# Optimization experiments

Hardware: AMD Instinct MI355X
Metric: run time of the kernel (lower is better)

## Reference

```python
import jax, jax.numpy as jnp
import numpy as np
from jax import lax

N = 64            # n_channels
L = 5             # n_layers
CLS = 12          # n_classes
B = 262144        # batch
NUM_MZI = N * (N - 1) // 2
C_HALF = 0.7071067811865476  # sqrt(0.5)
RESP = 0.8        # photodiode_responsivity
SENS = 0.001      # sensitivity
GAMMA = 0.05      # fwhm / 2

# MZI pair indices in the same order as the torch double loop (i, then j>i)
_II, _JJ = np.triu_indices(N, k=1)
_II = jnp.asarray(_II, dtype=jnp.int32)
_JJ = jnp.asarray(_JJ, dtype=jnp.int32)


def construct_unitary(mzi_phases, output_phases):
    # mzi_phases: [NUM_MZI*2] interleaved (theta, phi); output_phases: [N]
    thetas = mzi_phases[0::2]
    phis = mzi_phases[1::2]

    def step(U, inp):
        i, j, theta, phi = inp
        ui = U[i]
        uj = U[j]
        e_phi = jnp.exp(1j * phi)
        e_theta = jnp.exp(1j * theta)
        new_i = C_HALF * ui + C_HALF * e_phi * uj
        new_j = C_HALF * e_theta * ui - C_HALF * e_theta * e_phi * uj
        U = U.at[i].set(new_i).at[j].set(new_j)
        return U, None

    U0 = jnp.eye(N, dtype=jnp.complex64)
    U, _ = lax.scan(step, U0, (_II, _JJ, thetas, phis))
    # output phase screen: diag(exp(i*phase)) @ U
    return jnp.exp(1j * output_phases)[:, None] * U


def nofu(field, beta_param, initial_detuning):
    beta = jax.nn.sigmoid(beta_param)                       # [N]
    input_power = jnp.abs(field) ** 2                       # [B, N]
    detuning = initial_detuning + SENS * RESP * beta * input_power
    transmission = GAMMA / (GAMMA + 1j * detuning)          # complex Lorentzian
    return jnp.sqrt(jax.nn.relu(1.0 - beta)) * field * transmission


def setup_inputs() -> dict:
    key = jax.random.key(0)
    ks = jax.random.split(key, 12)
    return {
        "x": jax.random.normal(ks[0], (B, N), dtype=jnp.float32),
        "mzi_phases": 0.1 * jax.random.normal(ks[1], (L, NUM_MZI * 2), dtype=jnp.float32),
        "output_phases": 0.1 * jax.random.normal(ks[2], (L, N), dtype=jnp.float32),
        "beta_param": 0.1 * jax.random.normal(ks[3], (L - 1, N), dtype=jnp.float32),
        "initial_detuning": 0.1 * jax.random.normal(ks[4], (L - 1, N), dtype=jnp.float32),
        "W1": 0.1 * jax.random.normal(ks[5], (2 * N, N), dtype=jnp.float32),
        "b1": jnp.zeros((2 * N,), dtype=jnp.float32),
        "W2": 0.1 * jax.random.normal(ks[6], (N, 2 * N), dtype=jnp.float32),
        "b2": jnp.zeros((N,), dtype=jnp.float32),
        "W3": 0.1 * jax.random.normal(ks[7], (CLS, N), dtype=jnp.float32),
        "b3": jnp.zeros((CLS,), dtype=jnp.float32),
    }


def reference(x, mzi_phases, output_phases, beta_param, initial_detuning,
              W1, b1, W2, b2, W3, b3):
    field = x.astype(jnp.complex64)                         # [B, N]
    for l in range(L):
        U = construct_unitary(mzi_phases[l], output_phases[l])  # [N, N] complex
        field = jnp.einsum("ij,bj->bi", U, field)
        if l < L - 1:
            field = nofu(field, beta_param[l], initial_detuning[l])
    power = jnp.abs(field) ** 2                             # [B, N] real
    h = jax.nn.relu(power @ W1.T + b1)
    h = jax.nn.relu(h @ W2.T + b2)
    return h @ W3.T + b3                                    # [B, CLS]
```

## Files before the change

kernel.cpp:

```cpp
#include <hip/hip_runtime.h>
#include <math.h>


#define NN 64
#define LL 5
#define NMZI 2016
#define C_HALF 0.7071067811865476f
#define GAMMA_ 0.05f
#define SENSRESP 0.0008f

#define AH_SHORTS   114688
#define FLOAT_BYTE  458752
#define PSEG_BYTE   466944
#define FROW 136

typedef short short8 __attribute__((ext_vector_type(8)));
typedef float f32x4  __attribute__((ext_vector_type(4)));

union U4S8 { uint4 u; short8 s; };

#define MFMA16(a, b, c) __builtin_amdgcn_mfma_f32_16x16x32_bf16((a), (b), (c), 0, 0, 0)

__device__ __forceinline__ unsigned short f2bf(float f) {
    unsigned u = __float_as_uint(f);
    unsigned r = u + 0x7fffu + ((u >> 16) & 1u);
    return (unsigned short)(r >> 16);
}
__device__ __forceinline__ float bf2f(unsigned short h) {
    return __uint_as_float(((unsigned)h) << 16);
}
__device__ __forceinline__ unsigned rnebits(float v) {
    unsigned u = __float_as_uint(v);
    return u + 0x7fffu + ((u >> 16) & 1u);
}
__device__ __forceinline__ unsigned permhi16(unsigned a, unsigned b) {
    return __builtin_amdgcn_perm(a, b, 0x03020706);
}
__device__ __forceinline__ void split4(const float* v, uint2& hi, uint2& lo) {
    unsigned r0 = rnebits(v[0]), r1 = rnebits(v[1]);
    unsigned r2 = rnebits(v[2]), r3 = rnebits(v[3]);
    hi.x = permhi16(r0, r1);
    hi.y = permhi16(r2, r3);
    float l0 = v[0] - __uint_as_float(r0 & 0xffff0000u);
    float l1 = v[1] - __uint_as_float(r1 & 0xffff0000u);
    float l2 = v[2] - __uint_as_float(r2 & 0xffff0000u);
    float l3 = v[3] - __uint_as_float(r3 & 0xffff0000u);
    lo.x = permhi16(__float_as_uint(l0), __float_as_uint(l1));
    lo.y = permhi16(__float_as_uint(l2), __float_as_uint(l3));
}
__device__ __forceinline__ int afrag_off(int l, int m, int k) {
    return ((((l * 8 + (m >> 4)) * 4 + (k >> 5)) << 9)
          + ((((k >> 3) & 3) * 16 + (m & 15)) << 3) + (k & 7));
}

template<int I0, int I1>
__device__ __forceinline__ void run_scan(const float cs[][4], float* ur, float* ui)
{
    int m = 0;
    #pragma unroll
    for (int i = I0; i < I1; ++i) {
        #pragma unroll
        for (int j = i + 1; j < NN; ++j) {
            float cph = cs[m][0], sph = cs[m][1];
            float cct = cs[m][2], cst = cs[m][3];
            float tr = cph * ur[j] - sph * ui[j];
            float ti = cph * ui[j] + sph * ur[j];
            float ar = ur[i] + tr, ai = ui[i] + ti;
            float sr = ur[i] - tr, si = ui[i] - ti;
            ur[i] = C_HALF * ar;
            ui[i] = C_HALF * ai;
            ur[j] = cct * sr - cst * si;
            ui[j] = cct * si + cst * sr;
            ++m;
        }
    }
}

__global__ __launch_bounds__(64) void build_seg(
    const float* __restrict__ mzi, float2* __restrict__ Pg)
{
    const int b = blockIdx.x;
    const int l = b >> 2, s = b & 3;
    const int c = threadIdx.x;

    __shared__ float cs[531][4];
    const int M0s[5] = {0, 531, 1026, 1488, 2016};
    const int m0 = M0s[s], cnt = M0s[s + 1] - m0;

    for (int t = c; t < cnt; t += 64) {
        int m = m0 + t;
        float th = mzi[l * 2 * NMZI + 2 * m];
        float ph = mzi[l * 2 * NMZI + 2 * m + 1];
        float sth, cth, sph, cph;
        sincosf(th, &sth, &cth);
        sincosf(ph, &sph, &cph);
        cs[t][0] = cph; cs[t][1] = sph;
        cs[t][2] = C_HALF * cth; cs[t][3] = C_HALF * sth;
    }
    __syncthreads();

    float ur[NN], ui[NN];
    #pragma unroll
    for (int r = 0; r < NN; ++r) { ur[r] = (r == c) ? 1.f : 0.f; ui[r] = 0.f; }

    switch (s) {
        case 0: run_scan<0,  9>(cs, ur, ui); break;
        case 1: run_scan<9, 19>(cs, ur, ui); break;
        case 2: run_scan<19,31>(cs, ur, ui); break;
        default:run_scan<31,63>(cs, ur, ui); break;
    }

    float2* P = Pg + ((size_t)(l * 4 + s) << 12) + (c << 6);
    #pragma unroll
    for (int r = 0; r < NN; ++r) P[r] = make_float2(ur[r], ui[r]);
}

__device__ __forceinline__ void cpass(const float2* A, const float2* Bm,
                                      int rq, int c, float2* y)
{
    #pragma unroll
    for (int r = 0; r < 16; ++r) y[r] = make_float2(0.f, 0.f);
    #pragma unroll 2
    for (int k = 0; k < 64; ++k) {
        float2 x = Bm[c * 65 + k];
        #pragma unroll
        for (int r = 0; r < 16; ++r) {
            float2 a = A[k * 65 + 16 * rq + r];
            y[r].x = fmaf(a.x, x.x, fmaf(-a.y, x.y, y[r].x));
            y[r].y = fmaf(a.x, x.y, fmaf( a.y, x.x, y[r].y));
        }
    }
}

__device__ __forceinline__ void store_split(unsigned short* AH, unsigned short* AL,
                                            int l, int m, int k, float v)
{
    int o = afrag_off(l, m, k);
    unsigned short h = f2bf(v);
    AH[o] = h;
    AL[o] = f2bf(v - bf2f(h));
}

__global__ __launch_bounds__(256) void build_combine(
    const float2* __restrict__ Pg, const float* __restrict__ oph,
    unsigned short* __restrict__ AH)
{
    unsigned short* AL = AH + AH_SHORTS;
    extern __shared__ float cl[];
    float2* B0 = (float2*)cl;
    float2* B1 = B0 + 4160;
    float2* B2 = B1 + 4160;
    float2* B3 = B2 + 4160;
    float2* ocs = B3 + 4160;

    const int l = blockIdx.x;
    const int tid = threadIdx.x;
    const int rq = tid >> 6, c = tid & 63;

    const float2* Pgl = Pg + ((size_t)l << 14);
    #pragma unroll
    for (int sb = 0; sb < 4; ++sb) {
        float2* Bb = B0 + sb * 4160;
        #pragma unroll
        for (int i = 0; i < 16; ++i) {
            int idx = tid + i * 256;
            Bb[(idx >> 6) * 65 + (idx & 63)] = Pgl[(sb << 12) + idx];
        }
    }
    if (tid < NN) {
        float sp, cp; sincosf(oph[l * NN + tid], &sp, &cp);
        ocs[tid] = make_float2(cp, sp);
    }
    __syncthreads();

    float2 t1[16], t2[16];
    cpass(B1, B0, rq, c, t1);
    cpass(B3, B2, rq, c, t2);
    __syncthreads();
    #pragma unroll
    for (int r = 0; r < 16; ++r) {
        B0[c * 65 + 16 * rq + r] = t1[r];
        B2[c * 65 + 16 * rq + r] = t2[r];
    }
    __syncthreads();

    float2 u[16];
    cpass(B2, B0, rq, c, u);

    #pragma unroll
    for (int r = 0; r < 16; ++r) {
        int mr = 16 * rq + r;
        float2 oc = ocs[mr];
        float vr = oc.x * u[r].x - oc.y * u[r].y;
        float vi = oc.x * u[r].y + oc.y * u[r].x;
        store_split(AH, AL, l, mr,      c,      vr);
        store_split(AH, AL, l, mr,      c + 64, -vi);
        store_split(AH, AL, l, mr + 64, c,      vi);
        store_split(AH, AL, l, mr + 64, c + 64, vr);
    }
}

__global__ void prep_weights(const float* __restrict__ W1,
                             const float* __restrict__ W2,
                             const float* __restrict__ W3,
                             const float* __restrict__ beta_param,
                             const float* __restrict__ det0,
                             unsigned short* __restrict__ AH)
{
    unsigned short* AL = AH + AH_SHORTS;
    float* fbase = (float*)((char*)AH + FLOAT_BYTE);
    float* nofuF = fbase;
    float* W3T   = fbase + 1024;

    int idx = blockIdx.x * 256 + threadIdx.x;
    if (idx < 8192) {
        int mm = idx >> 6, k = idx & 63;
        float v = W1[idx];
        unsigned short h = f2bf(v);
        int o = afrag_off(5, mm, k);
        AH[o] = h; AL[o] = f2bf(v - bf2f(h));
    } else if (idx < 16384) {
        int t = idx - 8192;
        int mm = t >> 7, k = t & 127;
        float v = W2[t];
        unsigned short h = f2bf(v);
        int o = afrag_off(6, mm, k);
        AH[o] = h; AL[o] = f2bf(v - bf2f(h));
    } else if (idx < 17152) {
        int t = idx - 16384;
        int r = t >> 6, j = t & 63;
        W3T[j * 12 + r] = W3[t];
    } else if (idx < 17408) {
        int t = idx - 17152;
        float bp = beta_param[t];
        float beta = 1.f / (1.f + expf(-bp));
        float* p = nofuF + t * 4;
        p[0] = SENSRESP * beta;
        p[1] = sqrtf(fmaxf(1.f - beta, 0.f)) * GAMMA_;
        p[2] = det0[t];
        p[3] = 0.f;
    }
}

template<int K4, bool PAIR>
__device__ __forceinline__ void mm_block(
    const unsigned short* __restrict__ AH, const unsigned short* __restrict__ AL,
    const unsigned short* Fh, const unsigned short* Fl,
    int slot, int mt0, int lane, int q, const int* brow,
    f32x4* acc0, f32x4* acc1)
{
    #pragma unroll
    for (int Kt = 0; Kt < K4; ++Kt) {
        int off0 = (((slot * 8 + mt0) * 4 + Kt) << 9);
        U4S8 ah0, al0, ah1, al1;
        ah0.u = ((const uint4*)(AH + off0))[lane];
        al0.u = ((const uint4*)(AL + off0))[lane];
        if (PAIR) {
            ah1.u = ((const uint4*)(AH + off0 + 8192))[lane];
            al1.u = ((const uint4*)(AL + off0 + 8192))[lane];
        }
        #pragma unroll
        for (int t = 0; t < 4; ++t) {
            short8 bh = *(const short8*)&Fh[brow[t] + 32 * Kt + 8 * q];
            short8 bl = *(const short8*)&Fl[brow[t] + 32 * Kt + 8 * q];
            acc0[t] = MFMA16(ah0.s, bh, acc0[t]);
            acc0[t] = MFMA16(ah0.s, bl, acc0[t]);
            acc0[t] = MFMA16(al0.s, bh, acc0[t]);
            if (PAIR) {
                acc1[t] = MFMA16(ah1.s, bh, acc1[t]);
                acc1[t] = MFMA16(ah1.s, bl, acc1[t]);
                acc1[t] = MFMA16(al1.s, bh, acc1[t]);
            }
        }
    }
}

__global__ __launch_bounds__(256, 4) void ficonn_main(
    const float* __restrict__ x,
    const float* __restrict__ b1,
    const float* __restrict__ b2,
    const float* __restrict__ b3,
    const unsigned short* __restrict__ AH,
    const float4* __restrict__ nofuC,
    const float* __restrict__ W3T,
    float* __restrict__ out)
{
    const unsigned short* AL = AH + AH_SHORTS;
    extern __shared__ unsigned short Fdyn[];
    unsigned short* Fh = Fdyn;
    unsigned short* Fl = Fdyn + 64 * FROW;

    const int tid  = threadIdx.x;
    const int lane = tid & 63;
    const int w    = __builtin_amdgcn_readfirstlane(tid >> 6);
    const int mp   = w;
    const int n16  = lane & 15, q = lane >> 4;
    const int base = blockIdx.x * 64;

    {
        const float4* x4 = (const float4*)(x + (size_t)base * 64);
        #pragma unroll
        for (int it = 0; it < 4; ++it) {
            int idx = tid + it * 256;
            int j4 = idx & 15, ss = idx >> 4;
            float4 v4 = x4[idx];
            float vv[4] = {v4.x, v4.y, v4.z, v4.w};
            uint2 hi, lo; split4(vv, hi, lo);
            *(uint2*)&Fh[ss * FROW + 4 * j4] = hi;
            *(uint2*)&Fl[ss * FROW + 4 * j4] = lo;
        }
    }
    __syncthreads();

    int brow[4];
    #pragma unroll
    for (int t = 0; t < 4; ++t) brow[t] = (16 * t + n16) * FROW;
    const int kw = 16 * mp + 4 * q;

    #pragma unroll 1
    for (int l = 0; l < 5; ++l) {
        f32x4 acc0[4], acc1[4];
        #pragma unroll
        for (int t = 0; t < 4; ++t)
            #pragma unroll
            for (int r = 0; r < 4; ++r) { acc0[t][r] = 0.f; acc1[t][r] = 0.f; }

        if (l == 0) mm_block<2, true>(AH, AL, Fh, Fl, 0, mp, lane, q, brow, acc0, acc1);
        else        mm_block<4, true>(AH, AL, Fh, Fl, l, mp, lane, q, brow, acc0, acc1);
        __syncthreads();

        if (l < 4) {
            float4 nc[4];
            #pragma unroll
            for (int r = 0; r < 4; ++r) nc[r] = nofuC[l * 64 + kw + r];
            #pragma unroll
            for (int t = 0; t < 4; ++t) {
                float wr[4], wi[4];
                #pragma unroll
                for (int r = 0; r < 4; ++r) {
                    float yr = acc0[t][r], yi = acc1[t][r];
                    float4 c = nc[r];
                    float p   = fmaf(yr, yr, yi * yi);
                    float det = fmaf(c.x, p, c.z);
                    float sc  = c.y * __builtin_amdgcn_rcpf(fmaf(det, det, GAMMA_ * GAMMA_));
                    float tr = sc * GAMMA_, ti = sc * det;
                    wr[r] = fmaf(tr, yr,  ti * yi);
                    wi[r] = fmaf(tr, yi, -ti * yr);
                }
                uint2 hi, lo;
                split4(wr, hi, lo);
                *(uint2*)&Fh[brow[t] + kw] = hi;
                *(uint2*)&Fl[brow[t] + kw] = lo;
                split4(wi, hi, lo);
                *(uint2*)&Fh[brow[t] + kw + 64] = hi;
                *(uint2*)&Fl[brow[t] + kw + 64] = lo;
            }
        } else {
            #pragma unroll
            for (int t = 0; t < 4; ++t) {
                float pw[4];
                #pragma unroll
                for (int r = 0; r < 4; ++r)
                    pw[r] = fmaf(acc0[t][r], acc0[t][r], acc1[t][r] * acc1[t][r]);
                uint2 hi, lo;
                split4(pw, hi, lo);
                *(uint2*)&Fh[brow[t] + kw] = hi;
                *(uint2*)&Fl[brow[t] + kw] = lo;
            }
        }
        __syncthreads();
    }

    {
        f32x4 acc0[4], acc1[4];
        #pragma unroll
        for (int t = 0; t < 4; ++t)
            #pragma unroll
            for (int r = 0; r < 4; ++r) { acc0[t][r] = 0.f; acc1[t][r] = 0.f; }

        mm_block<2, true>(AH, AL, Fh, Fl, 5, mp, lane, q, brow, acc0, acc1);
        __syncthreads();

        float4 bb0 = *(const float4*)&b1[kw];
        float4 bb1 = *(const float4*)&b1[kw + 64];
        #pragma unroll
        for (int t = 0; t < 4; ++t) {
            float h0[4], h1v[4];
            #pragma unroll
            for (int r = 0; r < 4; ++r) {
                h0[r]  = fmaxf(acc0[t][r] + ((const float*)&bb0)[r], 0.f);
                h1v[r] = fmaxf(acc1[t][r] + ((const float*)&bb1)[r], 0.f);
            }
            uint2 hi, lo;
            split4(h0, hi, lo);
            *(uint2*)&Fh[brow[t] + kw] = hi;
            *(uint2*)&Fl[brow[t] + kw] = lo;
            split4(h1v, hi, lo);
            *(uint2*)&Fh[brow[t] + kw + 64] = hi;
            *(uint2*)&Fl[brow[t] + kw + 64] = lo;
        }
        __syncthreads();
    }

    {
        f32x4 acc0[4], acc1[4];
        #pragma unroll
        for (int t = 0; t < 4; ++t)
            #pragma unroll
            for (int r = 0; r < 4; ++r) acc0[t][r] = 0.f;

        mm_block<4, false>(AH, AL, Fh, Fl, 6, mp, lane, q, brow, acc0, acc1);
        __syncthreads();

        float4 bb = *(const float4*)&b2[kw];
        #pragma unroll
        for (int t = 0; t < 4; ++t) {
            float h[4];
            #pragma unroll
            for (int r = 0; r < 4; ++r)
                h[r] = fmaxf(acc0[t][r] + ((const float*)&bb)[r], 0.f);
            uint2 hi, lo;
            split4(h, hi, lo);
            *(uint2*)&Fh[brow[t] + kw] = hi;
            *(uint2*)&Fl[brow[t] + kw] = lo;
        }
        __syncthreads();
    }

    {
        const int n  = tid & 63;
        const int rg = __builtin_amdgcn_readfirstlane(tid >> 6);
        float o0 = b3[3 * rg], o1 = b3[3 * rg + 1], o2 = b3[3 * rg + 2];
        const unsigned short* rh = &Fh[n * FROW];
        const unsigned short* rl = &Fl[n * FROW];
        #pragma unroll
        for (int kc = 0; kc < 8; ++kc) {
            uint4 ph = *(const uint4*)&rh[8 * kc];
            uint4 pl = *(const uint4*)&rl[8 * kc];
            unsigned hu[4] = {ph.x, ph.y, ph.z, ph.w};
            unsigned lu[4] = {pl.x, pl.y, pl.z, pl.w};
            #pragma unroll
            for (int e = 0; e < 4; ++e) {
                int k = 8 * kc + 2 * e;
                float ha = __uint_as_float(hu[e] << 16)
                         + __uint_as_float(lu[e] << 16);
                float hb = __uint_as_float(hu[e] & 0xffff0000u)
                         + __uint_as_float(lu[e] & 0xffff0000u);
                const float* wa = W3T + k * 12 + 3 * rg;
                const float* wb = wa + 12;
                o0 = fmaf(wa[0], ha, fmaf(wb[0], hb, o0));
                o1 = fmaf(wa[1], ha, fmaf(wb[1], hb, o1));
                o2 = fmaf(wa[2], ha, fmaf(wb[2], hb, o2));
            }
        }
        float* op = out + (size_t)(base + n) * 12 + 3 * rg;
        op[0] = o0; op[1] = o1; op[2] = o2;
    }
}

extern "C" void kernel_launch(void* const* d_in, const int* in_sizes, int n_in,
                              void* d_out, int out_size, void* d_ws, size_t ws_size,
                              hipStream_t stream)
{
    const float* x    = (const float*)d_in[0];
    const float* mzi  = (const float*)d_in[1];
    const float* oph  = (const float*)d_in[2];
    const float* beta = (const float*)d_in[3];
    const float* det0 = (const float*)d_in[4];
    const float* W1   = (const float*)d_in[5];
    const float* b1   = (const float*)d_in[6];
    const float* W2   = (const float*)d_in[7];
    const float* b2   = (const float*)d_in[8];
    const float* W3   = (const float*)d_in[9];
    const float* b3   = (const float*)d_in[10];
    float* out = (float*)d_out;

    unsigned short* AH = (unsigned short*)d_ws;
    float* fbase = (float*)((char*)d_ws + FLOAT_BYTE);
    const float4* nofuC = (const float4*)fbase;
    const float* W3T = fbase + 1024;
    float2* Pg = (float2*)((char*)d_ws + PSEG_BYTE);

    const int B = in_sizes[0] / NN;
    const int blocks = B / 64;
    const size_t main_lds = 2u * 64u * FROW * sizeof(unsigned short);
    const size_t comb_lds = (4u * 4160u + 64u) * sizeof(float2);

    hipLaunchKernelGGL(build_seg, dim3(20), dim3(64), 0, stream, mzi, Pg);
    hipLaunchKernelGGL(prep_weights, dim3(68), dim3(256), 0, stream,
                       W1, W2, W3, beta, det0, AH);
    hipLaunchKernelGGL(build_combine, dim3(LL), dim3(256), comb_lds, stream,
                       Pg, oph, AH);
    hipLaunchKernelGGL(ficonn_main, dim3(blocks), dim3(512 / 2), main_lds, stream,
                       x, b1, b2, b3, AH, nofuC, W3T, out);
}
```

Measured before the change: 326.8 us.

## Swizzle LDS activation layout, use packed bf16 convert, raise occupancy

Replaces the padded LDS row layout (136 shorts per row) with a 256-byte row and an XOR swizzle on the column byte offset, which reduces LDS footprint to 32 KB. The goal is to avoid bank conflicts without padding and to allow more resident blocks, so launch bounds go from 4 to 5 blocks per SIMD. It also swaps the manual round-to-nearest-even bit manipulation in the hi/lo bf16 split for the hardware v_cvt_pk_bf16_f32 instruction. The tighter launch bound may force register spilling.

After: 414.5 us. +26.8%, slower.

```diff
diff --git a/kernel.cpp b/kernel.cpp
--- a/kernel.cpp
+++ b/kernel.cpp
@@ -12,7 +12,6 @@
 #define AH_SHORTS   114688
 #define FLOAT_BYTE  458752
 #define PSEG_BYTE   466944
-#define FROW 136
 
 typedef short short8 __attribute__((ext_vector_type(8)));
 typedef float f32x4  __attribute__((ext_vector_type(4)));
@@ -29,24 +28,20 @@
 __device__ __forceinline__ float bf2f(unsigned short h) {
     return __uint_as_float(((unsigned)h) << 16);
 }
-__device__ __forceinline__ unsigned rnebits(float v) {
-    unsigned u = __float_as_uint(v);
-    return u + 0x7fffu + ((u >> 16) & 1u);
-}
-__device__ __forceinline__ unsigned permhi16(unsigned a, unsigned b) {
-    return __builtin_amdgcn_perm(a, b, 0x03020706);
+__device__ __forceinline__ unsigned cvtpk(float a, float b) {
+    unsigned r;
+    asm("v_cvt_pk_bf16_f32 %0, %1, %2" : "=v"(r) : "v"(a), "v"(b));
+    return r;
 }
 __device__ __forceinline__ void split4(const float* v, uint2& hi, uint2& lo) {
-    unsigned r0 = rnebits(v[0]), r1 = rnebits(v[1]);
-    unsigned r2 = rnebits(v[2]), r3 = rnebits(v[3]);
-    hi.x = permhi16(r0, r1);
-    hi.y = permhi16(r2, r3);
-    float l0 = v[0] - __uint_as_float(r0 & 0xffff0000u);
-    float l1 = v[1] - __uint_as_float(r1 & 0xffff0000u);
-    float l2 = v[2] - __uint_as_float(r2 & 0xffff0000u);
-    float l3 = v[3] - __uint_as_float(r3 & 0xffff0000u);
-    lo.x = permhi16(__float_as_uint(l0), __float_as_uint(l1));
-    lo.y = permhi16(__float_as_uint(l2), __float_as_uint(l3));
+    hi.x = cvtpk(v[0], v[1]);
+    hi.y = cvtpk(v[2], v[3]);
+    float l0 = v[0] - __uint_as_float(hi.x << 16);
+    float l1 = v[1] - __uint_as_float(hi.x & 0xffff0000u);
+    float l2 = v[2] - __uint_as_float(hi.y << 16);
+    float l3 = v[3] - __uint_as_float(hi.y & 0xffff0000u);
+    lo.x = cvtpk(l0, l1);
+    lo.y = cvtpk(l2, l3);
 }
 __device__ __forceinline__ int afrag_off(int l, int m, int k) {
     return ((((l * 8 + (m >> 4)) * 4 + (k >> 5)) << 9)
@@ -246,7 +241,7 @@
 __device__ __forceinline__ void mm_block(
     const unsigned short* __restrict__ AH, const unsigned short* __restrict__ AL,
     const unsigned short* Fh, const unsigned short* Fl,
-    int slot, int mt0, int lane, int q, const int* brow,
+    int slot, int mt0, int lane, int q, int x0, const int* rowb,
     f32x4* acc0, f32x4* acc1)
 {
     #pragma unroll
@@ -259,10 +254,11 @@
             ah1.u = ((const uint4*)(AH + off0 + 8192))[lane];
             al1.u = ((const uint4*)(AL + off0 + 8192))[lane];
         }
+        const int cb = (64 * Kt + 16 * q) ^ x0;
         #pragma unroll
         for (int t = 0; t < 4; ++t) {
-            short8 bh = *(const short8*)&Fh[brow[t] + 32 * Kt + 8 * q];
-            short8 bl = *(const short8*)&Fl[brow[t] + 32 * Kt + 8 * q];
+            short8 bh = *(const short8*)((const char*)Fh + rowb[t] + cb);
+            short8 bl = *(const short8*)((const char*)Fl + rowb[t] + cb);
             acc0[t] = MFMA16(ah0.s, bh, acc0[t]);
             acc0[t] = MFMA16(ah0.s, bl, acc0[t]);
             acc0[t] = MFMA16(al0.s, bh, acc0[t]);
@@ -275,7 +271,7 @@
     }
 }
 
-__global__ __launch_bounds__(256, 4) void ficonn_main(
+__global__ __launch_bounds__(256, 5) void ficonn_main(
     const float* __restrict__ x,
     const float* __restrict__ b1,
     const float* __restrict__ b2,
@@ -288,7 +284,7 @@
     const unsigned short* AL = AH + AH_SHORTS;
     extern __shared__ unsigned short Fdyn[];
     unsigned short* Fh = Fdyn;
-    unsigned short* Fl = Fdyn + 64 * FROW;
+    unsigned short* Fl = Fdyn + 8192;
 
     const int tid  = threadIdx.x;
     const int lane = tid & 63;
@@ -306,16 +302,19 @@
             float4 v4 = x4[idx];
             float vv[4] = {v4.x, v4.y, v4.z, v4.w};
             uint2 hi, lo; split4(vv, hi, lo);
-            *(uint2*)&Fh[ss * FROW + 4 * j4] = hi;
-            *(uint2*)&Fl[ss * FROW + 4 * j4] = lo;
+            int off = (ss << 8) + ((8 * j4) ^ ((ss & 7) << 4));
+            *(uint2*)((char*)Fh + off) = hi;
+            *(uint2*)((char*)Fl + off) = lo;
         }
     }
     __syncthreads();
 
-    int brow[4];
-    #pragma unroll
-    for (int t = 0; t < 4; ++t) brow[t] = (16 * t + n16) * FROW;
-    const int kw = 16 * mp + 4 * q;
+    const int x0 = (n16 & 7) << 4;
+    int rowb[4];
+    #pragma unroll
+    for (int t = 0; t < 4; ++t) rowb[t] = (16 * t + n16) << 8;
+    const int kw  = 16 * mp + 4 * q;
+    const int cwr = (32 * mp + 8 * q) ^ x0;
 
     #pragma unroll 1
     for (int l = 0; l < 5; ++l) {
@@ -325,8 +324,8 @@
             #pragma unroll
             for (int r = 0; r < 4; ++r) { acc0[t][r] = 0.f; acc1[t][r] = 0.f; }
 
-        if (l == 0) mm_block<2, true>(AH, AL, Fh, Fl, 0, mp, lane, q, brow, acc0, acc1);
-        else        mm_block<4, true>(AH, AL, Fh, Fl, l, mp, lane, q, brow, acc0, acc1);
+        if (l == 0) mm_block<2, true>(AH, AL, Fh, Fl, 0, mp, lane, q, x0, rowb, acc0, acc1);
+        else        mm_block<4, true>(AH, AL, Fh, Fl, l, mp, lane, q, x0, rowb, acc0, acc1);
         __syncthreads();
 
         if (l < 4) {
@@ -349,11 +348,11 @@
                 }
                 uint2 hi, lo;
                 split4(wr, hi, lo);
-                *(uint2*)&Fh[brow[t] + kw] = hi;
-                *(uint2*)&Fl[brow[t] + kw] = lo;
+                *(uint2*)((char*)Fh + rowb[t] + cwr) = hi;
+                *(uint2*)((char*)Fl + rowb[t] + cwr) = lo;
                 split4(wi, hi, lo);
-                *(uint2*)&Fh[brow[t] + kw + 64] = hi;
-                *(uint2*)&Fl[brow[t] + kw + 64] = lo;
+                *(uint2*)((char*)Fh + rowb[t] + cwr + 128) = hi;
+                *(uint2*)((char*)Fl + rowb[t] + cwr + 128) = lo;
             }
         } else {
             #pragma unroll
@@ -364,8 +363,8 @@
                     pw[r] = fmaf(acc0[t][r], acc0[t][r], acc1[t][r] * acc1[t][r]);
                 uint2 hi, lo;
                 split4(pw, hi, lo);
-                *(uint2*)&Fh[brow[t] + kw] = hi;
-                *(uint2*)&Fl[brow[t] + kw] = lo;
+                *(uint2*)((char*)Fh + rowb[t] + cwr) = hi;
+                *(uint2*)((char*)Fl + rowb[t] + cwr) = lo;
             }
         }
         __syncthreads();
@@ -378,7 +377,7 @@
             #pragma unroll
             for (int r = 0; r < 4; ++r) { acc0[t][r] = 0.f; acc1[t][r] = 0.f; }
 
-        mm_block<2, true>(AH, AL, Fh, Fl, 5, mp, lane, q, brow, acc0, acc1);
+        mm_block<2, true>(AH, AL, Fh, Fl, 5, mp, lane, q, x0, rowb, acc0, acc1);
         __syncthreads();
 
         float4 bb0 = *(const float4*)&b1[kw];
@@ -393,11 +392,11 @@
             }
             uint2 hi, lo;
             split4(h0, hi, lo);
-            *(uint2*)&Fh[brow[t] + kw] = hi;
-            *(uint2*)&Fl[brow[t] + kw] = lo;
+            *(uint2*)((char*)Fh + rowb[t] + cwr) = hi;
+            *(uint2*)((char*)Fl + rowb[t] + cwr) = lo;
             split4(h1v, hi, lo);
-            *(uint2*)&Fh[brow[t] + kw + 64] = hi;
-            *(uint2*)&Fl[brow[t] + kw + 64] = lo;
+            *(uint2*)((char*)Fh + rowb[t] + cwr + 128) = hi;
+            *(uint2*)((char*)Fl + rowb[t] + cwr + 128) = lo;
         }
         __syncthreads();
     }
@@ -409,7 +408,7 @@
             #pragma unroll
             for (int r = 0; r < 4; ++r) acc0[t][r] = 0.f;
 
-        mm_block<4, false>(AH, AL, Fh, Fl, 6, mp, lane, q, brow, acc0, acc1);
+        mm_block<4, false>(AH, AL, Fh, Fl, 6, mp, lane, q, x0, rowb, acc0, acc1);
         __syncthreads();
 
         float4 bb = *(const float4*)&b2[kw];
@@ -421,8 +420,8 @@
                 h[r] = fmaxf(acc0[t][r] + ((const float*)&bb)[r], 0.f);
             uint2 hi, lo;
             split4(h, hi, lo);
-            *(uint2*)&Fh[brow[t] + kw] = hi;
-            *(uint2*)&Fl[brow[t] + kw] = lo;
+            *(uint2*)((char*)Fh + rowb[t] + cwr) = hi;
+            *(uint2*)((char*)Fl + rowb[t] + cwr) = lo;
         }
         __syncthreads();
     }
@@ -431,12 +430,14 @@
         const int n  = tid & 63;
         const int rg = __builtin_amdgcn_readfirstlane(tid >> 6);
         float o0 = b3[3 * rg], o1 = b3[3 * rg + 1], o2 = b3[3 * rg + 2];
-        const unsigned short* rh = &Fh[n * FROW];
-        const unsigned short* rl = &Fl[n * FROW];
+        const char* rh = (const char*)Fh + (n << 8);
+        const char* rl = (const char*)Fl + (n << 8);
+        const int xr = (n & 7) << 4;
         #pragma unroll
         for (int kc = 0; kc < 8; ++kc) {
-            uint4 ph = *(const uint4*)&rh[8 * kc];
-            uint4 pl = *(const uint4*)&rl[8 * kc];
+            int cb = (16 * kc) ^ xr;
+            uint4 ph = *(const uint4*)(rh + cb);
+            uint4 pl = *(const uint4*)(rl + cb);
             unsigned hu[4] = {ph.x, ph.y, ph.z, ph.w};
             unsigned lu[4] = {pl.x, pl.y, pl.z, pl.w};
             #pragma unroll
@@ -483,7 +484,7 @@
 
     const int B = in_sizes[0] / NN;
     const int blocks = B / 64;
-    const size_t main_lds = 2u * 64u * FROW * sizeof(unsigned short);
+    const size_t main_lds = 32768;
     const size_t comb_lds = (4u * 4160u + 64u) * sizeof(float2);
 
     hipLaunchKernelGGL(build_seg, dim3(20), dim3(64), 0, stream, mzi, Pg);
@@ -491,6 +492,6 @@
                        W1, W2, W3, beta, det0, AH);
     hipLaunchKernelGGL(build_combine, dim3(LL), dim3(256), comb_lds, stream,
                        Pg, oph, AH);
-    hipLaunchKernelGGL(ficonn_main, dim3(blocks), dim3(512 / 2), main_lds, stream,
+    hipLaunchKernelGGL(ficonn_main, dim3(blocks), dim3(256), main_lds, stream,
                        x, b1, b2, b3, AH, nofuC, W3T, out);
 }
```
